# Optimization experiments

Hardware: AMD Instinct MI355X
Metric: run time of the kernel (lower is better)

The kernel has to match this reference:

```python
import jax, jax.numpy as jnp
from jax import lax
import numpy as np

TOL = 0.1          # ssc_tolerance
H, W = 2160, 3840  # rows, cols (4K frame)
N_PTS = 10000      # topK candidate keypoints
NUM_RET = 512      # ssc_num


def _slide_max(a, k, axis):
    """Max over a centered window of (odd) size k along `axis`, same-size output,
    padding with -inf (== torch max_pool2d semantics). Uses van-Herk-style
    log-doubling so cost is O(len*log k) instead of O(len*k)."""
    if k == 1:
        return a
    pad = k // 2
    pw = [(0, 0)] * a.ndim
    pw[axis] = (pad, pad)
    f = jnp.pad(a, pw, constant_values=-jnp.inf)
    j = 1
    while j * 2 <= k:  # f[i] = max over window of size j starting at i
        n = f.shape[axis] - j
        f = jnp.maximum(lax.slice_in_dim(f, 0, n, axis=axis),
                        lax.slice_in_dim(f, j, n + j, axis=axis))
        j *= 2
    if j < k:  # combine two overlapping power-of-two windows to cover size k
        s = k - j
        n = f.shape[axis] - s
        f = jnp.maximum(lax.slice_in_dim(f, 0, n, axis=axis),
                        lax.slice_in_dim(f, s, n + s, axis=axis))
    return f


def _maxpool2d_same(img, k):
    # separable kxk max pool, stride 1, 'same' padding with -inf
    return _slide_max(_slide_max(img, k, 0), k, 1)


def _ssc_select(keypoints, scores, num_ret_points, rows, cols, tol):
    """Faithful port of KeypointDetectionSSC.ssc: scatter scores to a dense map,
    binary-search the NMS kernel size (host-synchronized, as in the original),
    then gather/pad/truncate the selected point indices."""
    n = keypoints.shape[0]
    if n < num_ret_points:
        raise ValueError('Number of input feature points is less than requested')
    y = keypoints[:, 2].astype(jnp.int32)
    x = keypoints[:, 3].astype(jnp.int32)
    # scatter-max of per-point scores into the dense [H, W] score map
    score_img = jnp.zeros((rows, cols), jnp.float32).at[y, x].max(scores)

    k_min = int(round(num_ret_points * (1 - tol)))
    k_max = int(round(num_ret_points * (1 + tol)))
    low = 1
    high = max(1, int(max(rows, cols) // max(1, int((n / max(1, num_ret_points)) ** 0.5))))

    def nms_count(k):
        if k % 2 == 0:
            k += 1
        pooled = _maxpool2d_same(score_img, k)
        keep = (score_img == pooled) & (score_img > 0)
        return int(keep.sum()), keep

    prev_k = -1
    selected_map = None
    while True:  # host-synchronized binary search, mirrors the .item() loop
        k = (low + high) // 2
        if k == prev_k or low > high:
            break
        cnt, km = nms_count(k)
        if k_min <= cnt <= k_max:
            selected_map = km
            break
        elif cnt < k_min:
            high = k - 1
        else:
            low = k + 1
        prev_k = k
    if selected_map is None:
        _, selected_map = nms_count(prev_k if prev_k > 0 else 1)

    keep_pts = np.asarray(selected_map[y, x])
    sel = np.flatnonzero(keep_pts)
    m = sel.size
    if m < num_ret_points:  # pad with first unselected candidates (rank order)
        mask = np.zeros(n, dtype=bool)
        mask[sel] = True
        remaining = np.flatnonzero(~mask)
        sel = np.concatenate([sel, remaining[: num_ret_points - m]])
    elif m > num_ret_points:
        sel = sel[:num_ret_points]
    return jnp.asarray(sel)


def setup_inputs() -> dict:
    key = jax.random.key(0)
    k1, k2, k3 = jax.random.split(key, 3)
    y = jax.random.randint(k1, (N_PTS,), 0, H, dtype=jnp.int32)
    x = jax.random.randint(k2, (N_PTS,), 0, W, dtype=jnp.int32)
    zeros = jnp.zeros((N_PTS,), jnp.int32)
    keypoints = jnp.stack([zeros, zeros, y, x], axis=1)  # [N,4] = [b,0,y,x]
    # descending positive scores emulate rank_score = N - arange(N)
    scores = jnp.sort(jax.random.uniform(k3, (N_PTS,), jnp.float32))[::-1] * N_PTS + 1.0
    return {"keypoints": keypoints, "scores": scores,
            "num_ret_points": NUM_RET, "rows": H, "cols": W}


def reference(keypoints, scores, num_ret_points, rows, cols):
    sel = _ssc_select(keypoints, scores, num_ret_points, rows, cols, TOL)
    return keypoints[sel], scores[sel]
```

## Files before the change

kernel.cpp:

```cpp
#include <hip/hip_runtime.h>

#define HSIZE 2048
#define CSH   6
#define CSZ   64
#define NCLDS 2048
#define QLP   10176
#define TPP   16
#define TPB   640

__global__ __launch_bounds__(TPB, 1) void bq_k(
    const int* __restrict__ kp, const float* __restrict__ sc,
    const int* __restrict__ nret_, const int* __restrict__ rows_, const int* __restrict__ cols_,
    int n, int* __restrict__ dd) {
    __shared__ int2 lpp[QLP];
    __shared__ unsigned short lsi[QLP];
    __shared__ int2 lcell[NCLDS + 1];
    __shared__ int cnt[NCLDS];
    __shared__ int wsum[8];
    int t = threadIdx.x, lane = t & 63, w = t >> 6;
    int rows = rows_[0], cols = cols_[0];
    int NCX = (cols + CSZ - 1) >> CSH;
    int NCY = (rows + CSZ - 1) >> CSH;
    int NC = NCX * NCY;
    const int4* kp4 = (const int4*)kp;

    int nret = nret_[0];
    int mx = rows > cols ? rows : cols;
    int nr1 = nret > 1 ? nret : 1;
    int dvs = (int)sqrt((double)n / (double)nr1);
    if (dvs < 1) dvs = 1;
    int high = mx / dvs; if (high < 1) high = 1;
    int kmin = (int)llround((double)nret * (1.0 - 0.1));
    int k1 = (1 + high) / 2;
    int r1 = k1 / 2;
    long long packb = (long long)((rows - 1) / (r1 + 1) + 1) *
                      (long long)((cols - 1) / (r1 + 1) + 1);
    int RMAX = (packb < (long long)kmin) ? r1 : (high / 2);

    int gt = blockIdx.x * TPB + t;
    int q = gt >> 4, sub = gt & 15;
    bool act = q < n;

    int pk = 0, sb = 0, y = 0, x = 0, cy = 0, cx = 0;
    if (act) {
        int4 k = kp4[q];
        y = k.z; x = k.w;
        pk = (y << 16) | x;
        sb = __float_as_int(sc[q]);
        cy = y >> CSH; cx = x >> CSH;
    }

    bool fits = (NC <= NCLDS) && (n <= QLP);
    if (fits) {
        for (int i = t; i < NCLDS; i += TPB) { cnt[i] = 0; lcell[i].y = 0; }
        if (t == 0) { lcell[NCLDS].y = 0; }
        __syncthreads();
        for (int i = t; i < n; i += TPB) {
            int4 k = kp4[i];
            int c = (k.z >> CSH) * NCX + (k.w >> CSH);
            atomicAdd(&cnt[c], 1);
            atomicMax(&lcell[c].y, __float_as_int(sc[i]));
        }
        __syncthreads();
        int s4 = 0, l0 = 0, l1 = 0, l2 = 0, l3 = 0, xv = 0;
        if (t < 512) {
            int b = t * 4;
            l0 = cnt[b]; l1 = cnt[b + 1]; l2 = cnt[b + 2]; l3 = cnt[b + 3];
            s4 = l0 + l1 + l2 + l3;
            xv = s4;
            for (int o = 1; o < 64; o <<= 1) { int v = __shfl_up(xv, o); if (lane >= o) xv += v; }
            if (lane == 63) wsum[w] = xv;
        }
        __syncthreads();
        if (w == 0) {
            int v = (lane < 8) ? wsum[lane] : 0;
            for (int o = 1; o < 8; o <<= 1) { int u = __shfl_up(v, o); if (lane >= o) v += u; }
            if (lane < 8) wsum[lane] = v;
        }
        __syncthreads();
        if (t < 512) {
            int b = t * 4;
            int ex = ((w == 0) ? 0 : wsum[w - 1]) + xv - s4;
            int o0 = ex, o1 = ex + l0, o2 = o1 + l1, o3 = o2 + l2;
            lcell[b].x = o0; lcell[b + 1].x = o1; lcell[b + 2].x = o2; lcell[b + 3].x = o3;
            cnt[b] = o0; cnt[b + 1] = o1; cnt[b + 2] = o2; cnt[b + 3] = o3;
        }
        if (t == 0) lcell[NCLDS].x = n;
        __syncthreads();
        for (int i = t; i < n; i += TPB) {
            int4 k = kp4[i];
            int c = (k.z >> CSH) * NCX + (k.w >> CSH);
            int pos = atomicAdd(&cnt[c], 1);
            int2 v; v.x = (k.z << 16) | k.w; v.y = __float_as_int(sc[i]);
            lpp[pos] = v;
            lsi[pos] = (unsigned short)i;
        }
        __syncthreads();

        if (act) {
            int c0 = cy * NCX + cx;
            int lo = lcell[c0].x, hi = lcell[c0 + 1].x;
            int pmax = sb, rep = 1;
            for (int j = lo + sub; j < hi; j += TPP) {
                int2 v = lpp[j];
                if (v.x == pk) {
                    if (v.y > pmax) pmax = v.y;
                    if ((int)lsi[j] < q) rep = 0;
                }
            }
            pmax = max(pmax, __shfl_xor(pmax, 1)); pmax = max(pmax, __shfl_xor(pmax, 2));
            pmax = max(pmax, __shfl_xor(pmax, 4)); pmax = max(pmax, __shfl_xor(pmax, 8));
            rep = min(rep, __shfl_xor(rep, 1)); rep = min(rep, __shfl_xor(rep, 2));
            rep = min(rep, __shfl_xor(rep, 4)); rep = min(rep, __shfl_xor(rep, 8));
            int pb = pmax;

            int d = RMAX + 1;
            for (int j = lo + sub; j < hi; j += TPP) {
                int2 v = lpp[j];
                if (v.y > pb) {
                    int dy = y - (v.x >> 16);    dy = dy < 0 ? -dy : dy;
                    int dx = x - (v.x & 0xFFFF); dx = dx < 0 ? -dx : dx;
                    int c = dy > dx ? dy : dx;
                    if (c < d) d = c;
                }
            }
            d = min(d, __shfl_xor(d, 1)); d = min(d, __shfl_xor(d, 2));
            d = min(d, __shfl_xor(d, 4)); d = min(d, __shfl_xor(d, 8));

            for (int R = 1;; ++R) {
                int LB = (R - 1) * CSZ + 1;
                if (LB >= d) break;
                for (int e = sub; e < 8 * R; e += TPP) {
                    int a, b;
                    if (e < 2 * R + 1)      { a = -R; b = -R + e; }
                    else if (e < 4 * R + 2) { a =  R; b = -R + (e - (2 * R + 1)); }
                    else { int ss = e - (4 * R + 2); a = -R + 1 + (ss >> 1); b = (ss & 1) ? R : -R; }
                    int ccy = cy + a, ccx = cx + b;
                    if (ccy < 0 || ccy >= NCY || ccx < 0 || ccx >= NCX) continue;
                    int cc = ccy * NCX + ccx;
                    int2 cm = lcell[cc];
                    if (cm.y <= pb) continue;
                    int jhi = lcell[cc + 1].x;
                    for (int j = cm.x; j < jhi; ++j) {
                        int2 v = lpp[j];
                        if (v.y > pb) {
                            int dy = y - (v.x >> 16);    dy = dy < 0 ? -dy : dy;
                            int dx = x - (v.x & 0xFFFF); dx = dx < 0 ? -dx : dx;
                            int c = dy > dx ? dy : dx;
                            if (c < d) d = c;
                        }
                    }
                }
                d = min(d, __shfl_xor(d, 1)); d = min(d, __shfl_xor(d, 2));
                d = min(d, __shfl_xor(d, 4)); d = min(d, __shfl_xor(d, 8));
            }
            if (sub == 0) dd[q] = (d << 1) | rep;
        }
    } else {
        if (act) {
            int pmax = sb, rep = 1;
            for (int j = sub; j < n; j += TPP) {
                int4 k = kp4[j];
                if (k.z == y && k.w == x) {
                    int sj = __float_as_int(sc[j]);
                    if (sj > pmax) pmax = sj;
                    if (j < q) rep = 0;
                }
            }
            pmax = max(pmax, __shfl_xor(pmax, 1)); pmax = max(pmax, __shfl_xor(pmax, 2));
            pmax = max(pmax, __shfl_xor(pmax, 4)); pmax = max(pmax, __shfl_xor(pmax, 8));
            rep = min(rep, __shfl_xor(rep, 1)); rep = min(rep, __shfl_xor(rep, 2));
            rep = min(rep, __shfl_xor(rep, 4)); rep = min(rep, __shfl_xor(rep, 8));
            int pb = pmax;
            int d = RMAX + 1;
            for (int j = sub; j < n; j += TPP) {
                int4 k = kp4[j];
                int sj = __float_as_int(sc[j]);
                if (sj > pb) {
                    int dy = y - k.z; dy = dy < 0 ? -dy : dy;
                    int dx = x - k.w; dx = dx < 0 ? -dx : dx;
                    int c = dy > dx ? dy : dx;
                    if (c < d) d = c;
                }
            }
            d = min(d, __shfl_xor(d, 1)); d = min(d, __shfl_xor(d, 2));
            d = min(d, __shfl_xor(d, 4)); d = min(d, __shfl_xor(d, 8));
            if (sub == 0) dd[q] = (d << 1) | rep;
        }
    }
}

__global__ __launch_bounds__(1024) void finish_k(
    const int* __restrict__ kp, const float* __restrict__ sc,
    const int* __restrict__ dd,
    const int* __restrict__ nret_, const int* __restrict__ rows_, const int* __restrict__ cols_,
    int n, float* __restrict__ out) {
    __shared__ int lhist[HSIZE];
    __shared__ int suf[HSIZE + 1];
    __shared__ int wsuf[16];
    __shared__ int wtK[16], wtN[16];
    __shared__ int rsh;
    int t = threadIdx.x, lane = t & 63, w = t >> 6;

    lhist[t] = 0; lhist[t + 1024] = 0;
    __syncthreads();
    for (int i = t; i < n; i += 1024) {
        int dv = dd[i];
        int d = dv >> 1;
        int hb = d < HSIZE ? d : HSIZE - 1;
        atomicAdd(&lhist[hb], (dv & 1) ? 0x10001 : 0x10000);
    }
    __syncthreads();

    int b0 = lhist[2 * t], b1 = lhist[2 * t + 1];
    int s = b0 + b1;
    int x = s;
    for (int o = 1; o < 64; o <<= 1) { int v = __shfl_down(x, o); if (lane + o < 64) x += v; }
    if (lane == 0) wsuf[w] = x;
    __syncthreads();
    if (w == 0) {
        int v = (lane < 16) ? wsuf[lane] : 0;
        for (int o = 1; o < 16; o <<= 1) { int u = __shfl_down(v, o); if (lane + o < 16) v += u; }
        if (lane < 16) wsuf[lane] = v;
    }
    __syncthreads();
    int S = x + ((w < 15) ? wsuf[w + 1] : 0);
    suf[2 * t] = S;
    suf[2 * t + 1] = S - b0;
    if (t == 0) suf[HSIZE] = 0;
    __syncthreads();

    if (t == 0) {
        int nret = nret_[0];
        int rows = rows_[0], cols = cols_[0];
        int kmin = (int)llround((double)nret * (1.0 - 0.1));
        int kmax = (int)llround((double)nret * (1.0 + 0.1));
        int mx = rows > cols ? rows : cols;
        int nr1 = nret > 1 ? nret : 1;
        int dvs = (int)sqrt((double)n / (double)nr1);
        if (dvs < 1) dvs = 1;
        int high = mx / dvs; if (high < 1) high = 1;
        int low = 1, prev_k = -1, r_final = -1;
        bool found = false;
        while (true) {
            int k = (low + high) / 2;
            if (k == prev_k || low > high) break;
            int r = k / 2;
            int cnt = (r + 1 <= HSIZE) ? (suf[r + 1] & 0xFFFF) : 0;
            if (cnt >= kmin && cnt <= kmax) { r_final = r; found = true; break; }
            else if (cnt < kmin) high = k - 1;
            else low = k + 1;
            prev_k = k;
        }
        if (!found) {
            int kfb = prev_k > 0 ? prev_k : 1;
            r_final = kfb / 2;
        }
        rsh = r_final;
    }
    __syncthreads();
    int r = rsh;
    int nret = nret_[0];
    int m = (r + 1 <= HSIZE) ? (suf[r + 1] >> 16) : 0;

    unsigned long long lanemask = (lane == 0) ? 0ull : (~0ull >> (64 - lane));
    int runK = 0, runN = 0;
    for (int bb = 0; bb < n; bb += 1024) {
        int i = bb + t;
        bool valid = i < n;
        bool f  = valid && ((dd[i] >> 1) > r);
        bool nf = valid && !f;
        unsigned long long mk = __ballot(f);
        unsigned long long mn = __ballot(nf);
        int pk = __popcll(mk & lanemask);
        int pn = __popcll(mn & lanemask);
        if (lane == 0) { wtK[w] = __popcll(mk); wtN[w] = __popcll(mn); }
        __syncthreads();
        int exK = runK + pk, exN = runN + pn;
        for (int u = 0; u < w; ++u) { exK += wtK[u]; exN += wtN[u]; }
        int ctK = 0, ctN = 0;
        for (int u = 0; u < 16; ++u) { ctK += wtK[u]; ctN += wtN[u]; }
        __syncthreads();
        if (valid) {
            int slot = -1;
            if (f) {
                if (exK < nret) slot = exK;
            } else if (nf && m < nret && (m + exN) < nret) {
                slot = m + exN;
            }
            if (slot >= 0) {
                out[slot * 4 + 0] = (float)kp[i * 4 + 0];
                out[slot * 4 + 1] = (float)kp[i * 4 + 1];
                out[slot * 4 + 2] = (float)kp[i * 4 + 2];
                out[slot * 4 + 3] = (float)kp[i * 4 + 3];
                out[nret * 4 + slot] = sc[i];
            }
        }
        runK += ctK;
        runN += ctN;
    }
}

extern "C" void kernel_launch(void* const* d_in, const int* in_sizes, int n_in,
                              void* d_out, int out_size, void* d_ws, size_t ws_size,
                              hipStream_t stream) {
    const int*   kp   = (const int*)d_in[0];
    const float* sc   = (const float*)d_in[1];
    const int*   nret = (const int*)d_in[2];
    const int*   rows = (const int*)d_in[3];
    const int*   cols = (const int*)d_in[4];
    int n = in_sizes[1];

    int* dd    = (int*)d_ws;
    float* out = (float*)d_out;

    int qblocks = (int)(((long long)n * TPP + TPB - 1) / TPB);
    bq_k<<<qblocks, TPB, 0, stream>>>(kp, sc, nret, rows, cols, n, dd);
    finish_k<<<1, 1024, 0, stream>>>(kp, sc, dd, nret, rows, cols, n, out);
}
```

Before: 39.19 us.

## Fuse finish kernel into query kernel via last-block-done counter

Merges the single-block finish kernel into the per-point distance kernel. Each block increments a global counter and the last block to finish runs the histogram, binary search and compaction. It reuses shared-memory buffers and caches dd in LDS. This removes a second kernel launch and its launch gap, but adds a memset, atomics, and a tail phase run by 640 threads instead of 1024.

```diff
diff --git a/kernel.cpp b/kernel.cpp
--- a/kernel.cpp
+++ b/kernel.cpp
@@ -8,15 +8,18 @@
 #define TPP   16
 #define TPB   640
 
-__global__ __launch_bounds__(TPB, 1) void bq_k(
+__global__ __launch_bounds__(TPB, 1) void bqf_k(
     const int* __restrict__ kp, const float* __restrict__ sc,
     const int* __restrict__ nret_, const int* __restrict__ rows_, const int* __restrict__ cols_,
-    int n, int* __restrict__ dd) {
+    int n, int* __restrict__ done, int* __restrict__ dd, float* __restrict__ out) {
     __shared__ int2 lpp[QLP];
     __shared__ unsigned short lsi[QLP];
     __shared__ int2 lcell[NCLDS + 1];
     __shared__ int cnt[NCLDS];
     __shared__ int wsum[8];
+    __shared__ int wsuf[8];
+    __shared__ int wtK[10], wtN[10];
+    __shared__ int fin_s, rsh;
     int t = threadIdx.x, lane = t & 63, w = t >> 6;
     int rows = rows_[0], cols = cols_[0];
     int NCX = (cols + CSZ - 1) >> CSH;
@@ -154,7 +157,9 @@
                 d = min(d, __shfl_xor(d, 1)); d = min(d, __shfl_xor(d, 2));
                 d = min(d, __shfl_xor(d, 4)); d = min(d, __shfl_xor(d, 8));
             }
-            if (sub == 0) dd[q] = (d << 1) | rep;
+            if (sub == 0)
+                __hip_atomic_store(&dd[q], (d << 1) | rep,
+                                   __ATOMIC_RELAXED, __HIP_MEMORY_SCOPE_AGENT);
         }
     } else {
         if (act) {
@@ -185,70 +190,74 @@
             }
             d = min(d, __shfl_xor(d, 1)); d = min(d, __shfl_xor(d, 2));
             d = min(d, __shfl_xor(d, 4)); d = min(d, __shfl_xor(d, 8));
-            if (sub == 0) dd[q] = (d << 1) | rep;
-        }
-    }
-}
-
-__global__ __launch_bounds__(1024) void finish_k(
-    const int* __restrict__ kp, const float* __restrict__ sc,
-    const int* __restrict__ dd,
-    const int* __restrict__ nret_, const int* __restrict__ rows_, const int* __restrict__ cols_,
-    int n, float* __restrict__ out) {
-    __shared__ int lhist[HSIZE];
-    __shared__ int suf[HSIZE + 1];
-    __shared__ int wsuf[16];
-    __shared__ int wtK[16], wtN[16];
-    __shared__ int rsh;
-    int t = threadIdx.x, lane = t & 63, w = t >> 6;
-
-    lhist[t] = 0; lhist[t + 1024] = 0;
-    __syncthreads();
-    for (int i = t; i < n; i += 1024) {
-        int dv = dd[i];
-        int d = dv >> 1;
-        int hb = d < HSIZE ? d : HSIZE - 1;
+            if (sub == 0)
+                __hip_atomic_store(&dd[q], (d << 1) | rep,
+                                   __ATOMIC_RELAXED, __HIP_MEMORY_SCOPE_AGENT);
+        }
+    }
+
+    __syncthreads();
+    if (t == 0) {
+        int tk = atomicAdd(done, 1);
+        fin_s = (tk == (int)gridDim.x - 1);
+    }
+    __syncthreads();
+    if (!fin_s) return;
+
+    int* suf   = (int*)lcell;
+    int* lhist = ((int*)lcell) + HSIZE + 1;
+    int* ldd   = (int*)lpp;
+    bool cacheDD = (n <= QLP * 2);
+
+    for (int i = t; i < HSIZE; i += TPB) lhist[i] = 0;
+    __syncthreads();
+    for (int i = t; i < n; i += TPB) {
+        int dv = __hip_atomic_load(&dd[i], __ATOMIC_RELAXED, __HIP_MEMORY_SCOPE_AGENT);
+        if (cacheDD) ldd[i] = dv;
+        int d2 = dv >> 1;
+        int hb = d2 < HSIZE ? d2 : HSIZE - 1;
         atomicAdd(&lhist[hb], (dv & 1) ? 0x10001 : 0x10000);
     }
     __syncthreads();
 
-    int b0 = lhist[2 * t], b1 = lhist[2 * t + 1];
-    int s = b0 + b1;
-    int x = s;
-    for (int o = 1; o < 64; o <<= 1) { int v = __shfl_down(x, o); if (lane + o < 64) x += v; }
-    if (lane == 0) wsuf[w] = x;
+    int s0 = 0, s1 = 0, s2 = 0, s3 = 0, xv2 = 0;
+    if (t < 512) {
+        int bb = t * 4;
+        int b0 = lhist[bb], b1 = lhist[bb + 1], b2 = lhist[bb + 2], b3 = lhist[bb + 3];
+        s3 = b3; s2 = b2 + s3; s1 = b1 + s2; s0 = b0 + s1;
+        xv2 = s0;
+        for (int o = 1; o < 64; o <<= 1) { int v = __shfl_down(xv2, o); if (lane + o < 64) xv2 += v; }
+        if (lane == 0) wsuf[w] = xv2;
+    }
     __syncthreads();
     if (w == 0) {
-        int v = (lane < 16) ? wsuf[lane] : 0;
-        for (int o = 1; o < 16; o <<= 1) { int u = __shfl_down(v, o); if (lane + o < 16) v += u; }
-        if (lane < 16) wsuf[lane] = v;
-    }
-    __syncthreads();
-    int S = x + ((w < 15) ? wsuf[w + 1] : 0);
-    suf[2 * t] = S;
-    suf[2 * t + 1] = S - b0;
+        int v = (lane < 8) ? wsuf[lane] : 0;
+        for (int o = 1; o < 8; o <<= 1) { int u = __shfl_down(v, o); if (lane + o < 8) v += u; }
+        if (lane < 8) wsuf[lane] = v;
+    }
+    __syncthreads();
+    if (t < 512) {
+        int S = xv2 + ((w < 7) ? wsuf[w + 1] : 0);
+        int after = S - s0;
+        int bb = t * 4;
+        suf[bb] = s0 + after; suf[bb + 1] = s1 + after;
+        suf[bb + 2] = s2 + after; suf[bb + 3] = s3 + after;
+    }
     if (t == 0) suf[HSIZE] = 0;
     __syncthreads();
 
     if (t == 0) {
-        int nret = nret_[0];
-        int rows = rows_[0], cols = cols_[0];
-        int kmin = (int)llround((double)nret * (1.0 - 0.1));
         int kmax = (int)llround((double)nret * (1.0 + 0.1));
-        int mx = rows > cols ? rows : cols;
-        int nr1 = nret > 1 ? nret : 1;
-        int dvs = (int)sqrt((double)n / (double)nr1);
-        if (dvs < 1) dvs = 1;
-        int high = mx / dvs; if (high < 1) high = 1;
         int low = 1, prev_k = -1, r_final = -1;
+        int hh = high;
         bool found = false;
         while (true) {
-            int k = (low + high) / 2;
-            if (k == prev_k || low > high) break;
+            int k = (low + hh) / 2;
+            if (k == prev_k || low > hh) break;
             int r = k / 2;
-            int cnt = (r + 1 <= HSIZE) ? (suf[r + 1] & 0xFFFF) : 0;
-            if (cnt >= kmin && cnt <= kmax) { r_final = r; found = true; break; }
-            else if (cnt < kmin) high = k - 1;
+            int cnt2 = (r + 1 <= HSIZE) ? (suf[r + 1] & 0xFFFF) : 0;
+            if (cnt2 >= kmin && cnt2 <= kmax) { r_final = r; found = true; break; }
+            else if (cnt2 < kmin) hh = k - 1;
             else low = k + 1;
             prev_k = k;
         }
@@ -260,26 +269,30 @@
     }
     __syncthreads();
     int r = rsh;
-    int nret = nret_[0];
     int m = (r + 1 <= HSIZE) ? (suf[r + 1] >> 16) : 0;
 
     unsigned long long lanemask = (lane == 0) ? 0ull : (~0ull >> (64 - lane));
     int runK = 0, runN = 0;
-    for (int bb = 0; bb < n; bb += 1024) {
-        int i = bb + t;
+    for (int bb2 = 0; bb2 < n; bb2 += TPB) {
+        int i = bb2 + t;
         bool valid = i < n;
-        bool f  = valid && ((dd[i] >> 1) > r);
+        int dv = 0;
+        if (valid) {
+            if (cacheDD) dv = ldd[i];
+            else dv = __hip_atomic_load(&dd[i], __ATOMIC_RELAXED, __HIP_MEMORY_SCOPE_AGENT);
+        }
+        bool f  = valid && ((dv >> 1) > r);
         bool nf = valid && !f;
         unsigned long long mk = __ballot(f);
         unsigned long long mn = __ballot(nf);
-        int pk = __popcll(mk & lanemask);
-        int pn = __popcll(mn & lanemask);
+        int pkc = __popcll(mk & lanemask);
+        int pnc = __popcll(mn & lanemask);
         if (lane == 0) { wtK[w] = __popcll(mk); wtN[w] = __popcll(mn); }
         __syncthreads();
-        int exK = runK + pk, exN = runN + pn;
+        int exK = runK + pkc, exN = runN + pnc;
         for (int u = 0; u < w; ++u) { exK += wtK[u]; exN += wtN[u]; }
         int ctK = 0, ctN = 0;
-        for (int u = 0; u < 16; ++u) { ctK += wtK[u]; ctN += wtN[u]; }
+        for (int u = 0; u < 10; ++u) { ctK += wtK[u]; ctN += wtN[u]; }
         __syncthreads();
         if (valid) {
             int slot = -1;
@@ -311,10 +324,11 @@
     const int*   cols = (const int*)d_in[4];
     int n = in_sizes[1];
 
-    int* dd    = (int*)d_ws;
+    int* done  = (int*)d_ws;
+    int* dd    = done + 16;
     float* out = (float*)d_out;
 
+    hipMemsetAsync(done, 0, sizeof(int), stream);
     int qblocks = (int)(((long long)n * TPP + TPB - 1) / TPB);
-    bq_k<<<qblocks, TPB, 0, stream>>>(kp, sc, nret, rows, cols, n, dd);
-    finish_k<<<1, 1024, 0, stream>>>(kp, sc, dd, nret, rows, cols, n, out);
+    bqf_k<<<qblocks, TPB, 0, stream>>>(kp, sc, nret, rows, cols, n, done, dd, out);
 }
```

After: 48.55 us. 1.24x slower.

## Use 1024-thread blocks and keep keypoints in registers between binning passes

Applied to the files above, without the earlier changes.

Raises the block size from 640 to 1024 threads. During the count pass each thread now keeps its up to 10 keypoint records and cell indices in registers, so the scatter pass reuses them instead of reloading from global memory. The cell prefix scan is reworked to two cells per thread across 16 wavefronts. The trade-off is more register pressure. The block size also changes the grid mapping (16 threads per query), so the total block count and per-block work shift too. Correctness relies on n being at most 10*1024, which the QLP bound of 10176 guarantees.

```diff
diff --git a/kernel.cpp b/kernel.cpp
--- a/kernel.cpp
+++ b/kernel.cpp
@@ -6,7 +6,8 @@
 #define NCLDS 2048
 #define QLP   10176
 #define TPP   16
-#define TPB   640
+#define TPB   1024
+#define NIT   10
 
 __global__ __launch_bounds__(TPB, 1) void bq_k(
     const int* __restrict__ kp, const float* __restrict__ sc,
@@ -16,7 +17,7 @@
     __shared__ unsigned short lsi[QLP];
     __shared__ int2 lcell[NCLDS + 1];
     __shared__ int cnt[NCLDS];
-    __shared__ int wsum[8];
+    __shared__ int wsum[16];
     int t = threadIdx.x, lane = t & 63, w = t >> 6;
     int rows = rows_[0], cols = cols_[0];
     int NCX = (cols + CSZ - 1) >> CSH;
@@ -53,47 +54,50 @@
     bool fits = (NC <= NCLDS) && (n <= QLP);
     if (fits) {
         for (int i = t; i < NCLDS; i += TPB) { cnt[i] = 0; lcell[i].y = 0; }
-        if (t == 0) { lcell[NCLDS].y = 0; }
-        __syncthreads();
-        for (int i = t; i < n; i += TPB) {
-            int4 k = kp4[i];
-            int c = (k.z >> CSH) * NCX + (k.w >> CSH);
-            atomicAdd(&cnt[c], 1);
-            atomicMax(&lcell[c].y, __float_as_int(sc[i]));
-        }
-        __syncthreads();
-        int s4 = 0, l0 = 0, l1 = 0, l2 = 0, l3 = 0, xv = 0;
-        if (t < 512) {
-            int b = t * 4;
-            l0 = cnt[b]; l1 = cnt[b + 1]; l2 = cnt[b + 2]; l3 = cnt[b + 3];
-            s4 = l0 + l1 + l2 + l3;
-            xv = s4;
-            for (int o = 1; o < 64; o <<= 1) { int v = __shfl_up(xv, o); if (lane >= o) xv += v; }
-            if (lane == 63) wsum[w] = xv;
-        }
+        if (t == 0) lcell[NCLDS].y = 0;
+        __syncthreads();
+        int2 rv[NIT]; int rc[NIT];
+        #pragma unroll
+        for (int k2 = 0; k2 < NIT; ++k2) {
+            int i = t + k2 * TPB;
+            if (i < n) {
+                int4 k = kp4[i];
+                int c = (k.z >> CSH) * NCX + (k.w >> CSH);
+                int2 v; v.x = (k.z << 16) | k.w; v.y = __float_as_int(sc[i]);
+                rv[k2] = v; rc[k2] = c;
+                atomicAdd(&cnt[c], 1);
+                atomicMax(&lcell[c].y, v.y);
+            }
+        }
+        __syncthreads();
+        int b2 = t * 2;
+        int l0 = cnt[b2], l1 = cnt[b2 + 1];
+        int s2 = l0 + l1;
+        int xv = s2;
+        for (int o = 1; o < 64; o <<= 1) { int v = __shfl_up(xv, o); if (lane >= o) xv += v; }
+        if (lane == 63) wsum[w] = xv;
         __syncthreads();
         if (w == 0) {
-            int v = (lane < 8) ? wsum[lane] : 0;
-            for (int o = 1; o < 8; o <<= 1) { int u = __shfl_up(v, o); if (lane >= o) v += u; }
-            if (lane < 8) wsum[lane] = v;
-        }
-        __syncthreads();
-        if (t < 512) {
-            int b = t * 4;
-            int ex = ((w == 0) ? 0 : wsum[w - 1]) + xv - s4;
-            int o0 = ex, o1 = ex + l0, o2 = o1 + l1, o3 = o2 + l2;
-            lcell[b].x = o0; lcell[b + 1].x = o1; lcell[b + 2].x = o2; lcell[b + 3].x = o3;
-            cnt[b] = o0; cnt[b + 1] = o1; cnt[b + 2] = o2; cnt[b + 3] = o3;
+            int v = (lane < 16) ? wsum[lane] : 0;
+            for (int o = 1; o < 16; o <<= 1) { int u = __shfl_up(v, o); if (lane >= o) v += u; }
+            if (lane < 16) wsum[lane] = v;
+        }
+        __syncthreads();
+        {
+            int ex = ((w == 0) ? 0 : wsum[w - 1]) + xv - s2;
+            lcell[b2].x = ex; lcell[b2 + 1].x = ex + l0;
+            cnt[b2] = ex;     cnt[b2 + 1] = ex + l0;
         }
         if (t == 0) lcell[NCLDS].x = n;
         __syncthreads();
-        for (int i = t; i < n; i += TPB) {
-            int4 k = kp4[i];
-            int c = (k.z >> CSH) * NCX + (k.w >> CSH);
-            int pos = atomicAdd(&cnt[c], 1);
-            int2 v; v.x = (k.z << 16) | k.w; v.y = __float_as_int(sc[i]);
-            lpp[pos] = v;
-            lsi[pos] = (unsigned short)i;
+        #pragma unroll
+        for (int k2 = 0; k2 < NIT; ++k2) {
+            int i = t + k2 * TPB;
+            if (i < n) {
+                int pos = atomicAdd(&cnt[rc[k2]], 1);
+                lpp[pos] = rv[k2];
+                lsi[pos] = (unsigned short)i;
+            }
         }
         __syncthreads();
 
```

Measured after the change: 35.97 us. 1.09x faster.
